# Optimization experiments

Measured on AMD Instinct MI355X. Metric: run time of the kernel, lower is better.

## Reference

```python
import jax, jax.numpy as jnp
import numpy as np

B, H, W, C = 8, 64, 64, 128
G = 8
K = 3
STRIDE, PAD, DIL = 1, 1, 1
OS = 1.0
HID = 2 * C
C_OUT = C
EPS = 1e-5


def setup_inputs():
    key = jax.random.key(0)
    ks = jax.random.split(key, 16)

    def n(k, shape, s=0.02):
        return jax.random.normal(k, shape, dtype=jnp.float32) * s

    inp = jax.random.normal(ks[0], (B, H, W, C), dtype=jnp.float32)
    return {
        "inp": inp,
        "w_proj": n(ks[1], (C, C), 0.05),
        "b_proj": jnp.zeros((C,), jnp.float32),
        "dw_w": n(ks[2], (C, 1, K, K), 0.1),
        "dw_b": jnp.zeros((C,), jnp.float32),
        "gamma": jnp.ones((C,), jnp.float32),
        "beta": jnp.zeros((C,), jnp.float32),
        "w_off": n(ks[3], (G * K * K * 2, C), 0.02),
        "b_off": n(ks[4], (G * K * K * 2,), 0.02),
        "w_mask": n(ks[5], (G * K * K, C), 0.02),
        "b_mask": n(ks[6], (G * K * K,), 0.02),
        "w_fc1": n(ks[7], (HID, C), 0.05),
        "b_fc1": jnp.zeros((HID,), jnp.float32),
        "w_fc2": n(ks[8], (C_OUT, HID), 0.05),
        "b_fc2": jnp.zeros((C_OUT,), jnp.float32),
    }


def _dcnv3_core(x, offset, mask):
    # x: (B,H,W,C); offset: (B,H,W,G*P*2); mask: (B,H,W,G*P), softmaxed over P
    b, h, w, c = x.shape
    cg = c // G
    p = K * K
    xpad = jnp.pad(x, ((0, 0), (PAD, PAD), (PAD, PAD), (0, 0)))
    hp, wp = h + 2 * PAD, w + 2 * PAD
    hout = (hp - (DIL * (K - 1) + 1)) // STRIDE + 1
    wout = (wp - (DIL * (K - 1) + 1)) // STRIDE + 1
    # reference points, normalized by padded spatial dims (DCNv3 convention)
    base = (DIL * (K - 1)) // 2 + 0.5
    ref_y = (base + jnp.arange(hout, dtype=x.dtype) * STRIDE) / hp
    ref_x = (base + jnp.arange(wout, dtype=x.dtype) * STRIDE) / wp
    # dilation kernel grid; flatten with p = i*K + j (row-major over kernel)
    k_lin = jnp.arange(K, dtype=x.dtype) * DIL - (DIL * (K - 1)) // 2
    grid_y = jnp.repeat(k_lin / hp, K)   # (P,)
    grid_x = jnp.tile(k_lin / wp, K)     # (P,)
    off = offset.reshape(b, hout, wout, G, p, 2)  # last dim = (dx, dy)
    loc_x = ref_x[None, None, :, None, None] + grid_x * OS + off[..., 0] * OS / wp
    loc_y = ref_y[None, :, None, None, None] + grid_y * OS + off[..., 1] * OS / hp
    # normalized [0,1] -> pixel coords (grid_sample align_corners=False)
    px = loc_x * wp - 0.5
    py = loc_y * hp - 0.5
    x0 = jnp.floor(px)
    y0 = jnp.floor(py)
    wx = px - x0
    wy = py - y0
    x0i = x0.astype(jnp.int32)
    y0i = y0.astype(jnp.int32)
    xg = xpad.reshape(b, hp * wp, G, cg).transpose(0, 2, 1, 3)  # (B,G,HpWp,Cg)
    m_tot = hout * wout * p

    def bgp(t):  # (B,Hout,Wout,G,P) -> (B,G,M,1)
        return t.transpose(0, 3, 1, 2, 4).reshape(b, G, m_tot)[..., None]

    def gather(iy, ix):
        valid = ((iy >= 0) & (iy < hp) & (ix >= 0) & (ix < wp)).astype(x.dtype)
        flat = jnp.clip(iy, 0, hp - 1) * wp + jnp.clip(ix, 0, wp - 1)
        v = jnp.take_along_axis(xg, bgp(flat), axis=2)  # (B,G,M,Cg)
        return v * bgp(valid)  # zero padding outside

    wxr, wyr = bgp(wx), bgp(wy)
    val = (gather(y0i, x0i) * (1 - wyr) * (1 - wxr)
           + gather(y0i, x0i + 1) * (1 - wyr) * wxr
           + gather(y0i + 1, x0i) * wyr * (1 - wxr)
           + gather(y0i + 1, x0i + 1) * wyr * wxr)
    m = bgp(mask.reshape(b, hout, wout, G, p))
    out = (val * m).reshape(b, G, hout * wout, p, cg).sum(3)  # (B,G,N,Cg)
    return out.transpose(0, 2, 1, 3).reshape(b, hout, wout, G * cg)


def reference(inp, w_proj, b_proj, dw_w, dw_b, gamma, beta, w_off, b_off,
              w_mask, b_mask, w_fc1, b_fc1, w_fc2, b_fc2):
    bsz = inp.shape[0]
    x = inp @ w_proj.T + b_proj  # input_proj
    # offset/mask branch: depthwise conv -> BN (batch stats) -> GELU
    xc = inp.transpose(0, 3, 1, 2)  # NCHW
    y = jax.lax.conv_general_dilated(
        xc, dw_w, (1, 1), [((K - 1) // 2, (K - 1) // 2)] * 2,
        feature_group_count=C, dimension_numbers=("NCHW", "OIHW", "NCHW"))
    y = y + dw_b[None, :, None, None]
    mean = y.mean(axis=(0, 2, 3), keepdims=True)
    var = ((y - mean) ** 2).mean(axis=(0, 2, 3), keepdims=True)
    y = (y - mean) * jax.lax.rsqrt(var + EPS)
    y = y * gamma[None, :, None, None] + beta[None, :, None, None]
    x1 = jax.nn.gelu(y, approximate=False).transpose(0, 2, 3, 1)  # (B,H,W,C)
    offset = x1 @ w_off.T + b_off
    mask = x1 @ w_mask.T + b_mask
    mask = jax.nn.softmax(mask.reshape(bsz, H, W, G, K * K), axis=-1).reshape(bsz, H, W, -1)
    x = _dcnv3_core(x, offset, mask)
    # out_proj MLP
    hdn = jax.nn.gelu(x @ w_fc1.T + b_fc1, approximate=False)
    out = hdn @ w_fc2.T + b_fc2
    return out.transpose(0, 3, 1, 2)  # (B,C_out,H,W)
```

## Files before the change

### kernel.cpp

```cpp
#include <hip/hip_runtime.h>
#include <math.h>

#define NPOS  32768
#define CDIM  128
#define HS    64
#define WSZ   64

typedef __bf16 bf8_t  __attribute__((ext_vector_type(8)));
typedef float  f32x4  __attribute__((ext_vector_type(4)));

__device__ __forceinline__ float gelu_exact(float x) {
    return 0.5f * x * (1.0f + erff(x * 0.70710678118654752f));
}

__device__ __forceinline__ unsigned short bf16c(float v) {
    return __builtin_bit_cast(unsigned short, (__bf16)v);
}

__device__ __forceinline__ uint4 pack8hi(const float* v) {
    unsigned hh[8];
    #pragma unroll
    for (int i = 0; i < 8; ++i) hh[i] = (unsigned)bf16c(v[i]);
    return make_uint4(hh[0] | (hh[1] << 16), hh[2] | (hh[3] << 16),
                      hh[4] | (hh[5] << 16), hh[6] | (hh[7] << 16));
}

__device__ __forceinline__ float bfd(unsigned u) {
    return __builtin_bit_cast(float, u << 16);
}

__device__ __forceinline__ void ufma(float* acc, uint4 c, float wgt) {
    const unsigned* cc = (const unsigned*)&c;
    #pragma unroll
    for (int j = 0; j < 4; ++j) {
        acc[2 * j]     += __builtin_bit_cast(float, cc[j] << 16) * wgt;
        acc[2 * j + 1] += __builtin_bit_cast(float, cc[j] & 0xFFFF0000u) * wgt;
    }
}


__device__ void prep_body(
    int bid, int tid,
    unsigned short* __restrict__ xpad,
    const float* __restrict__ w0, const float* __restrict__ w1,
    const float* __restrict__ w2, const float* __restrict__ w3,
    const float* __restrict__ w4, unsigned short* __restrict__ wb)
{
    if (bid < 130) {
        int idx = bid * 256 + tid;
        if (idx < 33280) {
            int c8 = (idx & 15) * 8;
            int cell = idx >> 4;
            int b = cell / 260, r = cell % 260;
            int h, w;
            if (r < 66)       { h = 0;  w = r; }
            else if (r < 132) { h = 65; w = r - 66; }
            else { int rr = r - 132; h = 1 + (rr >> 1); w = (rr & 1) * 65; }
            size_t o = (((size_t)b * 66 + h) * 66 + w) * 128 + c8;
            *(uint4*)(xpad + o) = make_uint4(0u, 0u, 0u, 0u);
        }
    } else {
        int sub = (bid - 130) * 4 + (tid >> 6);
        int lane = tid & 63;
        int NT, K, local; unsigned short* out; bool hl; bool comb = false;
        const float* W = nullptr; int N = 0;
        if (sub < 32)       { NT = 8;  K = 128; out = wb;          local = sub;       hl = false; W = w0; N = 128; }
        else if (sub < 88)  { NT = 14; K = 128; out = wb + 16384;  local = sub - 32;  hl = false; comb = true; }
        else if (sub < 152) { NT = 16; K = 128; out = wb + 45056;  local = sub - 88;  hl = true;  W = w3; N = 256; }
        else                { NT = 8;  K = 256; out = wb + 110592; local = sub - 152; hl = true;  W = w4; N = 128; }
        int KC = K / 32;
        int unit = KC * NT * 512;
        int kc = local / NT, t = local % NT;
        int nt = t * 16 + (lane & 15);
        const float* Wp = W; int n = nt, Nv = N;
        if (comb) {
            if (t < 9) { Wp = w1; n = nt;       Nv = 144; }
            else       { Wp = w2; n = nt - 144; Nv = 72;  }
        }
        int kb = kc * 32 + (lane >> 4) * 8;
        size_t base = ((size_t)local * 64 + lane) * 8;
        #pragma unroll
        for (int i = 0; i < 8; ++i) {
            float v = (n < Nv) ? Wp[(size_t)n * K + kb + i] : 0.f;
            __bf16 h = (__bf16)v;
            out[base + i] = __builtin_bit_cast(unsigned short, h);
            if (hl) {
                __bf16 l = (__bf16)(v - (float)h);
                out[unit + base + i] = __builtin_bit_cast(unsigned short, l);
            }
        }
    }
}

__device__ void dwconv_body(
    int blk, int tid,
    const float* __restrict__ inp, const float* __restrict__ dww,
    const float* __restrict__ dwb, unsigned short* __restrict__ ydwb,
    float* __restrict__ psum, float* __restrict__ psq,
    unsigned short* __restrict__ inpf)
{
    int b = blk >> 6, h = blk & 63;
    int c4 = (tid & 31) * 4;
    int wg = tid >> 5;

    float wreg[4][9];
    #pragma unroll
    for (int cc = 0; cc < 4; ++cc)
        #pragma unroll
        for (int p = 0; p < 9; ++p)
            wreg[cc][p] = dww[(c4 + cc) * 9 + p];
    float bia[4];
    #pragma unroll
    for (int cc = 0; cc < 4; ++cc) bia[cc] = dwb[c4 + cc];

    float s4[4] = {0,0,0,0}, q4[4] = {0,0,0,0};
    const float* ibase = inp + (size_t)(b << 12) * CDIM;

    for (int i = 0; i < 8; ++i) {
        int w = wg + i * 8;
        float acc[4] = {bia[0], bia[1], bia[2], bia[3]};
        float4 ctr;
        #pragma unroll
        for (int ky = 0; ky < 3; ++ky) {
            int yy = h + ky - 1;
            if (yy < 0 || yy >= HS) continue;
            #pragma unroll
            for (int kx = 0; kx < 3; ++kx) {
                int xx = w + kx - 1;
                if (xx < 0 || xx >= WSZ) continue;
                float4 v = *(const float4*)(ibase + (size_t)(yy * 64 + xx) * CDIM + c4);
                if (ky == 1 && kx == 1) ctr = v;
                int p = ky * 3 + kx;
                acc[0] += v.x * wreg[0][p];
                acc[1] += v.y * wreg[1][p];
                acc[2] += v.z * wreg[2][p];
                acc[3] += v.w * wreg[3][p];
            }
        }
        int r = (b << 12) + h * 64 + w;
        ushort4 o;
        o.x = bf16c(acc[0]); o.y = bf16c(acc[1]);
        o.z = bf16c(acc[2]); o.w = bf16c(acc[3]);
        *(ushort4*)(ydwb + (size_t)r * CDIM + c4) = o;
        {
            int rt = r >> 4, kc = c4 >> 5;
            int lp = (r & 15) + ((c4 & 31) >> 3) * 16;
            int i0 = c4 & 7;
            unsigned u0 = (unsigned)bf16c(ctr.x) | ((unsigned)bf16c(ctr.y) << 16);
            unsigned u1 = (unsigned)bf16c(ctr.z) | ((unsigned)bf16c(ctr.w) << 16);
            *(uint2*)(inpf + ((size_t)rt * 4 + kc) * 512 + lp * 8 + i0) = make_uint2(u0, u1);
        }
        #pragma unroll
        for (int cc = 0; cc < 4; ++cc) { s4[cc] += acc[cc]; q4[cc] += acc[cc] * acc[cc]; }
    }

    __shared__ float ls[8][128], lq[8][128];
    #pragma unroll
    for (int cc = 0; cc < 4; ++cc) { ls[wg][c4 + cc] = s4[cc]; lq[wg][c4 + cc] = q4[cc]; }
    __syncthreads();
    if (tid < 128) {
        float s = 0.f, q = 0.f;
        #pragma unroll
        for (int r = 0; r < 8; ++r) { s += ls[r][tid]; q += lq[r][tid]; }
        psum[blk * 128 + tid] = s;
        psq [blk * 128 + tid] = q;
    }
}

__global__ __launch_bounds__(256) void k_pd(
    const float* __restrict__ inp, unsigned short* __restrict__ inpf,
    unsigned short* __restrict__ xpad,
    const float* __restrict__ w0, const float* __restrict__ w1,
    const float* __restrict__ w2, const float* __restrict__ w3,
    const float* __restrict__ w4, unsigned short* __restrict__ wb,
    const float* __restrict__ dww, const float* __restrict__ dwb,
    unsigned short* __restrict__ ydwb, float* __restrict__ psum,
    float* __restrict__ psq)
{
    int bid = blockIdx.x;
    if (bid < 184) prep_body(bid, threadIdx.x, xpad, w0, w1, w2, w3, w4, wb);
    else           dwconv_body(bid - 184, threadIdx.x, inp, dww, dwb, ydwb, psum, psq, inpf);
}

__global__ __launch_bounds__(256) void k_bnstats(
    const float* __restrict__ psum, const float* __restrict__ psq,
    const float* __restrict__ gamma, const float* __restrict__ beta,
    float* __restrict__ sc, float* __restrict__ sh)
{
    int c = blockIdx.x;
    int t = threadIdx.x;
    float s = psum[t * 128 + c] + psum[(t + 256) * 128 + c];
    float q = psq [t * 128 + c] + psq [(t + 256) * 128 + c];
    __shared__ float rs[256], rq[256];
    rs[t] = s; rq[t] = q; __syncthreads();
    for (int off = 128; off > 0; off >>= 1) {
        if (t < off) { rs[t] += rs[t + off]; rq[t] += rq[t + off]; }
        __syncthreads();
    }
    if (t == 0) {
        float mean = rs[0] * (1.0f / 32768.0f);
        float var  = rq[0] * (1.0f / 32768.0f) - mean * mean;
        float scale = gamma[c] * rsqrtf(var + 1e-5f);
        sc[c] = scale;
        sh[c] = beta[c] - mean * scale;
    }
}

__device__ void bngelu_body(
    int bid, int tid,
    const unsigned short* __restrict__ ydwb, const float* __restrict__ sc,
    const float* __restrict__ sh, unsigned short* __restrict__ dst)
{
    int idx = bid * 256 + tid;
    int r = idx >> 4, k8 = (idx & 15) * 8;
    uint4 yv = *(const uint4*)(ydwb + (size_t)r * 128 + k8);
    const unsigned* cc = (const unsigned*)&yv;
    float t[8];
    #pragma unroll
    for (int j = 0; j < 4; ++j) {
        t[2 * j]     = bfd(cc[j]);
        t[2 * j + 1] = __builtin_bit_cast(float, cc[j] & 0xFFFF0000u);
    }
    float s[8], h[8];
    *(float4*)(s)     = *(const float4*)(sc + k8);
    *(float4*)(s + 4) = *(const float4*)(sc + k8 + 4);
    *(float4*)(h)     = *(const float4*)(sh + k8);
    *(float4*)(h + 4) = *(const float4*)(sh + k8 + 4);
    #pragma unroll
    for (int i = 0; i < 8; ++i) t[i] = gelu_exact(t[i] * s[i] + h[i]);
    uint4 hi = pack8hi(t);
    int rt = r >> 4, kc = k8 >> 5, lp = (r & 15) + ((k8 & 31) >> 3) * 16;
    size_t base = ((size_t)rt * 4 + kc) * 512 + lp * 8;
    *(uint4*)(dst + base) = hi;
}

template<int KDIM, int NT_TOT, int NT_W, int MODE, int NV>
__device__ void fgemm_body(
    int bx, int by, int tid,
    const unsigned short* __restrict__ AF, const unsigned short* __restrict__ WF,
    const float* __restrict__ bias, float* __restrict__ C,
    const float* __restrict__ bias2, float* __restrict__ C2)
{
    constexpr int KC = KDIM / 32;
    int lane = tid & 63, w = tid >> 6;
    int rt0 = bx * 8 + w * 2;
    int t0 = by * NT_W;

    f32x4 acc[2][NT_W];
    #pragma unroll
    for (int rt = 0; rt < 2; ++rt)
        #pragma unroll
        for (int t = 0; t < NT_W; ++t) acc[rt][t] = (f32x4){0.f, 0.f, 0.f, 0.f};

    const bf8_t* Ab0 = (const bf8_t*)AF + (size_t)rt0 * KC * 64 + lane;
    const bf8_t* Ab1 = Ab0 + KC * 64;
    const bf8_t* WHp = (const bf8_t*)WF + lane;

    #pragma unroll
    for (int kc = 0; kc < KC; ++kc) {
        bf8_t a0h = Ab0[kc * 64];
        bf8_t a1h = Ab1[kc * 64];
        #pragma unroll
        for (int t = 0; t < NT_W; ++t) {
            int tg = t0 + t;
            if (tg < NT_TOT) {
                bf8_t wh = WHp[(kc * NT_TOT + tg) * 64];
                acc[0][t] = __builtin_amdgcn_mfma_f32_16x16x32_bf16(wh, a0h, acc[0][t], 0, 0, 0);
                acc[1][t] = __builtin_amdgcn_mfma_f32_16x16x32_bf16(wh, a1h, acc[1][t], 0, 0, 0);
            }
        }
    }

    #pragma unroll
    for (int rt = 0; rt < 2; ++rt) {
        if (MODE == 3) {
            unsigned short* Cp = (unsigned short*)C;
            int m = (rt0 + rt) * 16 + (lane & 15);
            int bb_ = m >> 12, hwm = m & 4095;
            size_t rowb = (((size_t)bb_ * 66 + (hwm >> 6) + 1) * 66 + (hwm & 63) + 1) * 128;
            #pragma unroll
            for (int t = 0; t < NT_W; ++t) {
                int tg = t0 + t;
                int nb = tg * 16 + ((lane >> 4) << 2);
                if (tg < NT_TOT) {
                    float4 bb = *(const float4*)(bias + nb);
                    f32x4 a = acc[rt][t];
                    ushort4 v;
                    v.x = bf16c(a[0] + bb.x); v.y = bf16c(a[1] + bb.y);
                    v.z = bf16c(a[2] + bb.z); v.w = bf16c(a[3] + bb.w);
                    *(ushort4*)(Cp + rowb + nb) = v;
                }
            }
        } else if (MODE == 4) {
            unsigned short* Co = (unsigned short*)C;
            unsigned short* Cm = (unsigned short*)C2;
            int m = (rt0 + rt) * 16 + (lane & 15);
            #pragma unroll
            for (int t = 0; t < NT_W; ++t) {
                int tg = t0 + t;
                if (tg < NT_TOT) {
                    int nb = tg * 16 + ((lane >> 4) << 2);
                    f32x4 a = acc[rt][t];
                    if (nb < 144) {
                        float4 bb = *(const float4*)(bias + nb);
                        ushort4 v;
                        v.x = bf16c(a[0] + bb.x); v.y = bf16c(a[1] + bb.y);
                        v.z = bf16c(a[2] + bb.z); v.w = bf16c(a[3] + bb.w);
                        *(ushort4*)(Co + (size_t)m * 144 + nb) = v;
                    } else {
                        int col = nb - 144;
                        if (col + 4 <= 72) {
                            float4 bb = *(const float4*)(bias2 + col);
                            ushort4 v;
                            v.x = bf16c(a[0] + bb.x); v.y = bf16c(a[1] + bb.y);
                            v.z = bf16c(a[2] + bb.z); v.w = bf16c(a[3] + bb.w);
                            *(ushort4*)(Cm + (size_t)m * 72 + col) = v;
                        }
                    }
                }
            }
        }
    }
}

template<int KDIM, int NT_TOT, int NT_W, int MODE, int NV>
__global__ __launch_bounds__(256) void k_fgemm(
    const unsigned short* __restrict__ AF, const unsigned short* __restrict__ WF,
    const float* __restrict__ bias, float* __restrict__ C,
    const float* __restrict__ bias2, float* __restrict__ C2)
{
    fgemm_body<KDIM, NT_TOT, NT_W, MODE, NV>(
        blockIdx.x, blockIdx.y, threadIdx.x, AF, WF, bias, C, bias2, C2);
}

__global__ __launch_bounds__(256) void k_bp(
    const unsigned short* __restrict__ ydwb, const float* __restrict__ sc,
    const float* __restrict__ sh, unsigned short* __restrict__ x1f,
    const unsigned short* __restrict__ inpf, const unsigned short* __restrict__ wprojf,
    const float* __restrict__ bproj, unsigned short* __restrict__ xpad)
{
    int bid = blockIdx.x;
    if (bid < 2048) {
        bngelu_body(bid, threadIdx.x, ydwb, sc, sh, x1f);
    } else {
        int pbid = bid - 2048;
        fgemm_body<128, 8, 4, 3, 128>(pbid & 255, pbid >> 8, threadIdx.x,
            inpf, wprojf, bproj, (float*)xpad, nullptr, nullptr);
    }
}

__global__ __launch_bounds__(256) void k_dcn(
    const unsigned short* __restrict__ xpad, const unsigned short* __restrict__ offs,
    const unsigned short* __restrict__ msk, unsigned short* __restrict__ dcnf)
{
    int u = blockIdx.x * 256 + threadIdx.x;
    int g = u & 7;
    int pos = u >> 3;
    int b = pos >> 12, hw = pos & 4095, h = hw >> 6, w = hw & 63;

    const unsigned short* ml = msk + (size_t)pos * 72 + g * 9;
    float e[9];
    float mx = -1e30f;
    #pragma unroll
    for (int p = 0; p < 9; ++p) { e[p] = bfd((unsigned)ml[p]); mx = fmaxf(mx, e[p]); }
    float ssum = 0.f;
    #pragma unroll
    for (int p = 0; p < 9; ++p) { e[p] = __expf(e[p] - mx); ssum += e[p]; }
    float inv = 1.0f / ssum;

    const unsigned short* ob = offs + (size_t)pos * 144 + g * 18;
    const unsigned short* xb = xpad + (size_t)b * 557568 + g * 16;

    float acc[16];
    #pragma unroll
    for (int i = 0; i < 16; ++i) acc[i] = 0.f;

    #pragma unroll
    for (int p = 0; p < 9; ++p) {
        unsigned dpair = *(const unsigned*)(ob + p * 2);
        float dx = bfd(dpair);
        float dy = __builtin_bit_cast(float, dpair & 0xFFFF0000u);
        float px = (float)(w + (p % 3)) + dx;
        float py = (float)(h + (p / 3)) + dy;
        float x0f = floorf(px), y0f = floorf(py);
        float wx = px - x0f, wy = py - y0f;
        int ix = (int)x0f, iy = (int)y0f;
        int ix0 = max(min(ix, 65), 0),     ix1 = max(min(ix + 1, 65), 0);
        int iy0 = max(min(iy, 65), 0),     iy1 = max(min(iy + 1, 65), 0);
        int r0 = iy0 * 66, r1 = iy1 * 66;

        float mp  = e[p] * inv;
        float w11 = wy * wx * mp;
        float w10 = wy * mp - w11;
        float w01 = wx * mp - w11;
        float w00 = mp - w01 - w10 - w11;

        const unsigned short* c00 = xb + (size_t)(r0 + ix0) * 128;
        const unsigned short* c01 = xb + (size_t)(r0 + ix1) * 128;
        const unsigned short* c10 = xb + (size_t)(r1 + ix0) * 128;
        const unsigned short* c11 = xb + (size_t)(r1 + ix1) * 128;

        uint4 a00 = *(const uint4*)(c00), b00 = *(const uint4*)(c00 + 8);
        uint4 a01 = *(const uint4*)(c01), b01 = *(const uint4*)(c01 + 8);
        uint4 a10 = *(const uint4*)(c10), b10 = *(const uint4*)(c10 + 8);
        uint4 a11 = *(const uint4*)(c11), b11 = *(const uint4*)(c11 + 8);

        ufma(acc,     a00, w00); ufma(acc + 8, b00, w00);
        ufma(acc,     a01, w01); ufma(acc + 8, b01, w01);
        ufma(acc,     a10, w10); ufma(acc + 8, b10, w10);
        ufma(acc,     a11, w11); ufma(acc + 8, b11, w11);
    }

    int rt = pos >> 4, kc = g >> 1;
    int lp0 = (pos & 15) + (g & 1) * 32;
    size_t fb = ((size_t)rt * 4 + kc) * 512 + (size_t)lp0 * 8;
    uint4 hiA = pack8hi(acc);
    uint4 hiB = pack8hi(acc + 8);
    *(uint4*)(dcnf + fb)       = hiA;
    *(uint4*)(dcnf + fb + 128) = hiB;
}

__global__ __launch_bounds__(512) void k_mlp(
    const unsigned short* __restrict__ dcnf, const unsigned short* __restrict__ wf1,
    const float* __restrict__ bfc1, const unsigned short* __restrict__ wf2,
    const float* __restrict__ bfc2, float* __restrict__ out)
{
    __shared__ unsigned short hid[4][16][264];
    int tid = threadIdx.x;
    int lane = tid & 63, w = tid >> 6;
    int pr = w & 1, chunk = w >> 1;
    int bp = blockIdx.x * 2 + pr;
    int rt0 = bp * 2;
    int m = lane & 15, hi4 = (lane >> 4) << 2;

    f32x4 acc[2][4];
    #pragma unroll
    for (int r = 0; r < 2; ++r)
        #pragma unroll
        for (int t = 0; t < 4; ++t) acc[r][t] = (f32x4){0.f, 0.f, 0.f, 0.f};
    const bf8_t* Ab0 = (const bf8_t*)dcnf + (size_t)rt0 * 4 * 64 + lane;
    const bf8_t* Ab1 = Ab0 + 4 * 64;
    const bf8_t* WH1 = (const bf8_t*)wf1 + lane;
    #pragma unroll
    for (int kc = 0; kc < 4; ++kc) {
        bf8_t a0 = Ab0[kc * 64];
        bf8_t a1 = Ab1[kc * 64];
        #pragma unroll
        for (int t = 0; t < 4; ++t) {
            int tg = chunk * 4 + t;
            bf8_t wh = WH1[(kc * 16 + tg) * 64];
            acc[0][t] = __builtin_amdgcn_mfma_f32_16x16x32_bf16(wh, a0, acc[0][t], 0, 0, 0);
            acc[1][t] = __builtin_amdgcn_mfma_f32_16x16x32_bf16(wh, a1, acc[1][t], 0, 0, 0);
        }
    }
    #pragma unroll
    for (int r = 0; r < 2; ++r) {
        #pragma unroll
        for (int t = 0; t < 4; ++t) {
            int nb = (chunk * 4 + t) * 16 + hi4;
            float4 bb = *(const float4*)(bfc1 + nb);
            ushort4 v;
            v.x = bf16c(gelu_exact(acc[r][t][0] + bb.x));
            v.y = bf16c(gelu_exact(acc[r][t][1] + bb.y));
            v.z = bf16c(gelu_exact(acc[r][t][2] + bb.z));
            v.w = bf16c(gelu_exact(acc[r][t][3] + bb.w));
            *(ushort4*)(&hid[pr * 2 + r][m][nb]) = v;
        }
    }

    __syncthreads();

    f32x4 acc2[2][2];
    #pragma unroll
    for (int r = 0; r < 2; ++r)
        #pragma unroll
        for (int t = 0; t < 2; ++t) acc2[r][t] = (f32x4){0.f, 0.f, 0.f, 0.f};
    const bf8_t* WH2 = (const bf8_t*)wf2 + lane;
    #pragma unroll
    for (int kc = 0; kc < 8; ++kc) {
        bf8_t ah0 = *(const bf8_t*)(&hid[pr * 2 + 0][m][kc * 32 + (lane >> 4) * 8]);
        bf8_t ah1 = *(const bf8_t*)(&hid[pr * 2 + 1][m][kc * 32 + (lane >> 4) * 8]);
        #pragma unroll
        for (int t = 0; t < 2; ++t) {
            int tg = chunk * 2 + t;
            bf8_t wh = WH2[(kc * 8 + tg) * 64];
            acc2[0][t] = __builtin_amdgcn_mfma_f32_16x16x32_bf16(ah0, wh, acc2[0][t], 0, 0, 0);
            acc2[1][t] = __builtin_amdgcn_mfma_f32_16x16x32_bf16(ah1, wh, acc2[1][t], 0, 0, 0);
        }
    }
    #pragma unroll
    for (int r = 0; r < 2; ++r) {
        int m4 = (rt0 + r) * 16 + hi4;
        int b = m4 >> 12, hw = m4 & 4095;
        #pragma unroll
        for (int t = 0; t < 2; ++t) {
            int n = (chunk * 2 + t) * 16 + m;
            float bb = bfc2[n];
            f32x4 a = acc2[r][t];
            float4 v = {a[0] + bb, a[1] + bb, a[2] + bb, a[3] + bb};
            *(float4*)(out + (((size_t)(b * 128 + n)) << 12) + hw) = v;
        }
    }
}

extern "C" void kernel_launch(void* const* d_in, const int* in_sizes, int n_in,
                              void* d_out, int out_size, void* d_ws, size_t ws_size,
                              hipStream_t stream)
{
    const float* inp   = (const float*)d_in[0];
    const float* wproj = (const float*)d_in[1];
    const float* bproj = (const float*)d_in[2];
    const float* dww   = (const float*)d_in[3];
    const float* dwb   = (const float*)d_in[4];
    const float* gamma = (const float*)d_in[5];
    const float* beta  = (const float*)d_in[6];
    const float* woff  = (const float*)d_in[7];
    const float* boff  = (const float*)d_in[8];
    const float* wmask = (const float*)d_in[9];
    const float* bmask = (const float*)d_in[10];
    const float* wfc1  = (const float*)d_in[11];
    const float* bfc1  = (const float*)d_in[12];
    const float* wfc2  = (const float*)d_in[13];
    const float* bfc2  = (const float*)d_in[14];
    float* out = (float*)d_out;
    float* ws  = (float*)d_ws;

    unsigned short* xpad = (unsigned short*)ws;
    unsigned short* offs = (unsigned short*)(ws + 2230272);
    unsigned short* inpf  = (unsigned short*)(ws + 9179136);
    unsigned short* dcnf  = (unsigned short*)(ws + 9179136);
    unsigned short* x1f   = (unsigned short*)(ws + 13373440);
    unsigned short* ydwb  = (unsigned short*)(ws + 15470592);
    unsigned short* msk = (unsigned short*)(ws + 17567744);
    float* psum = ws + 19927040;
    float* psq  = ws + 19992576;
    float* scs  = ws + 20058112;
    float* shs  = ws + 20058240;
    unsigned short* wfr = (unsigned short*)(ws + 20058368);

    unsigned short* wproj_f = wfr;
    unsigned short* womb_f  = wfr + 16384;
    unsigned short* wfc1_f  = wfr + 45056;
    unsigned short* wfc2_f  = wfr + 110592;

    k_pd<<<696, 256, 0, stream>>>(inp, inpf, xpad, wproj, woff, wmask, wfc1, wfc2,
                                  wfr, dww, dwb, ydwb, psum, psq);
    k_bnstats<<<128, 256, 0, stream>>>(psum, psq, gamma, beta, scs, shs);
    k_bp<<<2560, 256, 0, stream>>>(ydwb, scs, shs, x1f, inpf, wproj_f, bproj, xpad);
    k_fgemm<128, 14, 4, 4, 224><<<dim3(256, 4), 256, 0, stream>>>(x1f, womb_f, boff, (float*)offs, bmask, (float*)msk);
    k_dcn<<<1024, 256, 0, stream>>>(xpad, offs, msk, dcnf);
    k_mlp<<<512, 512, 0, stream>>>(dcnf, wfc1_f, bfc1, wfc2_f, bfc2, out);
}
```

Before: 91.89 us.

## Fuse offset/mask projection GEMM into the DCN sampling kernel via shared memory

Removes the separate offset/mask GEMM launch and computes each block's 32 positions of offset and mask logits with MFMA inside k_dcn, staging them in LDS instead of writing to and rereading from global memory. This cuts one kernel launch and the global round-trip of the 216-wide bf16 offset/mask tensors. In exchange, each DCN block now does GEMM work before a __syncthreads, with 4 waves each computing 7 N-tiles, and uses extra LDS.

```diff
diff --git a/kernel.cpp b/kernel.cpp
--- a/kernel.cpp
+++ b/kernel.cpp
@@ -238,8 +238,7 @@
 __device__ void fgemm_body(
     int bx, int by, int tid,
     const unsigned short* __restrict__ AF, const unsigned short* __restrict__ WF,
-    const float* __restrict__ bias, float* __restrict__ C,
-    const float* __restrict__ bias2, float* __restrict__ C2)
+    const float* __restrict__ bias, float* __restrict__ C)
 {
     constexpr int KC = KDIM / 32;
     int lane = tid & 63, w = tid >> 6;
@@ -291,46 +290,8 @@
                     *(ushort4*)(Cp + rowb + nb) = v;
                 }
             }
-        } else if (MODE == 4) {
-            unsigned short* Co = (unsigned short*)C;
-            unsigned short* Cm = (unsigned short*)C2;
-            int m = (rt0 + rt) * 16 + (lane & 15);
-            #pragma unroll
-            for (int t = 0; t < NT_W; ++t) {
-                int tg = t0 + t;
-                if (tg < NT_TOT) {
-                    int nb = tg * 16 + ((lane >> 4) << 2);
-                    f32x4 a = acc[rt][t];
-                    if (nb < 144) {
-                        float4 bb = *(const float4*)(bias + nb);
-                        ushort4 v;
-                        v.x = bf16c(a[0] + bb.x); v.y = bf16c(a[1] + bb.y);
-                        v.z = bf16c(a[2] + bb.z); v.w = bf16c(a[3] + bb.w);
-                        *(ushort4*)(Co + (size_t)m * 144 + nb) = v;
-                    } else {
-                        int col = nb - 144;
-                        if (col + 4 <= 72) {
-                            float4 bb = *(const float4*)(bias2 + col);
-                            ushort4 v;
-                            v.x = bf16c(a[0] + bb.x); v.y = bf16c(a[1] + bb.y);
-                            v.z = bf16c(a[2] + bb.z); v.w = bf16c(a[3] + bb.w);
-                            *(ushort4*)(Cm + (size_t)m * 72 + col) = v;
-                        }
-                    }
-                }
-            }
-        }
-    }
-}
-
-template<int KDIM, int NT_TOT, int NT_W, int MODE, int NV>
-__global__ __launch_bounds__(256) void k_fgemm(
-    const unsigned short* __restrict__ AF, const unsigned short* __restrict__ WF,
-    const float* __restrict__ bias, float* __restrict__ C,
-    const float* __restrict__ bias2, float* __restrict__ C2)
-{
-    fgemm_body<KDIM, NT_TOT, NT_W, MODE, NV>(
-        blockIdx.x, blockIdx.y, threadIdx.x, AF, WF, bias, C, bias2, C2);
+        }
+    }
 }
 
 __global__ __launch_bounds__(256) void k_bp(
@@ -345,30 +306,78 @@
     } else {
         int pbid = bid - 2048;
         fgemm_body<128, 8, 4, 3, 128>(pbid & 255, pbid >> 8, threadIdx.x,
-            inpf, wprojf, bproj, (float*)xpad, nullptr, nullptr);
+            inpf, wprojf, bproj, (float*)xpad);
     }
 }
 
 __global__ __launch_bounds__(256) void k_dcn(
-    const unsigned short* __restrict__ xpad, const unsigned short* __restrict__ offs,
-    const unsigned short* __restrict__ msk, unsigned short* __restrict__ dcnf)
-{
-    int u = blockIdx.x * 256 + threadIdx.x;
-    int g = u & 7;
-    int pos = u >> 3;
+    const unsigned short* __restrict__ x1f, const unsigned short* __restrict__ womb,
+    const float* __restrict__ boff, const float* __restrict__ bmask,
+    const unsigned short* __restrict__ xpad, unsigned short* __restrict__ dcnf)
+{
+    __shared__ unsigned short offs_l[32][148];
+    __shared__ unsigned short msk_l[32][76];
+    int tid = threadIdx.x;
+    int lane = tid & 63, wv = tid >> 6;
+    int rtl = wv & 1, chunk = wv >> 1;
+    int rt = blockIdx.x * 2 + rtl;
+
+    {
+        f32x4 acc[7];
+        #pragma unroll
+        for (int t = 0; t < 7; ++t) acc[t] = (f32x4){0.f, 0.f, 0.f, 0.f};
+        const bf8_t* Ab = (const bf8_t*)x1f + (size_t)rt * 4 * 64 + lane;
+        const bf8_t* WH = (const bf8_t*)womb + lane;
+        #pragma unroll
+        for (int kc = 0; kc < 4; ++kc) {
+            bf8_t ah = Ab[kc * 64];
+            #pragma unroll
+            for (int t = 0; t < 7; ++t) {
+                int tg = chunk * 7 + t;
+                bf8_t wh = WH[(kc * 14 + tg) * 64];
+                acc[t] = __builtin_amdgcn_mfma_f32_16x16x32_bf16(wh, ah, acc[t], 0, 0, 0);
+            }
+        }
+        int m = rtl * 16 + (lane & 15);
+        #pragma unroll
+        for (int t = 0; t < 7; ++t) {
+            int tg = chunk * 7 + t;
+            int nb = tg * 16 + ((lane >> 4) << 2);
+            f32x4 a = acc[t];
+            if (nb < 144) {
+                float4 bb = *(const float4*)(boff + nb);
+                ushort4 v;
+                v.x = bf16c(a[0] + bb.x); v.y = bf16c(a[1] + bb.y);
+                v.z = bf16c(a[2] + bb.z); v.w = bf16c(a[3] + bb.w);
+                *(ushort4*)(&offs_l[m][nb]) = v;
+            } else {
+                int col = nb - 144;
+                if (col + 4 <= 72) {
+                    float4 bb = *(const float4*)(bmask + col);
+                    ushort4 v;
+                    v.x = bf16c(a[0] + bb.x); v.y = bf16c(a[1] + bb.y);
+                    v.z = bf16c(a[2] + bb.z); v.w = bf16c(a[3] + bb.w);
+                    *(ushort4*)(&msk_l[m][col]) = v;
+                }
+            }
+        }
+    }
+    __syncthreads();
+
+    int g = tid & 7;
+    int lpos = tid >> 3;
+    int pos = blockIdx.x * 32 + lpos;
     int b = pos >> 12, hw = pos & 4095, h = hw >> 6, w = hw & 63;
 
-    const unsigned short* ml = msk + (size_t)pos * 72 + g * 9;
     float e[9];
     float mx = -1e30f;
     #pragma unroll
-    for (int p = 0; p < 9; ++p) { e[p] = bfd((unsigned)ml[p]); mx = fmaxf(mx, e[p]); }
+    for (int p = 0; p < 9; ++p) { e[p] = bfd((unsigned)msk_l[lpos][g * 9 + p]); mx = fmaxf(mx, e[p]); }
     float ssum = 0.f;
     #pragma unroll
     for (int p = 0; p < 9; ++p) { e[p] = __expf(e[p] - mx); ssum += e[p]; }
     float inv = 1.0f / ssum;
 
-    const unsigned short* ob = offs + (size_t)pos * 144 + g * 18;
     const unsigned short* xb = xpad + (size_t)b * 557568 + g * 16;
 
     float acc[16];
@@ -377,7 +386,7 @@
 
     #pragma unroll
     for (int p = 0; p < 9; ++p) {
-        unsigned dpair = *(const unsigned*)(ob + p * 2);
+        unsigned dpair = *(const unsigned*)(&offs_l[lpos][g * 18 + p * 2]);
         float dx = bfd(dpair);
         float dy = __builtin_bit_cast(float, dpair & 0xFFFF0000u);
         float px = (float)(w + (p % 3)) + dx;
@@ -411,9 +420,9 @@
         ufma(acc,     a11, w11); ufma(acc + 8, b11, w11);
     }
 
-    int rt = pos >> 4, kc = g >> 1;
+    int rto = pos >> 4, kc = g >> 1;
     int lp0 = (pos & 15) + (g & 1) * 32;
-    size_t fb = ((size_t)rt * 4 + kc) * 512 + (size_t)lp0 * 8;
+    size_t fb = ((size_t)rto * 4 + kc) * 512 + (size_t)lp0 * 8;
     uint4 hiA = pack8hi(acc);
     uint4 hiB = pack8hi(acc + 8);
     *(uint4*)(dcnf + fb)       = hiA;
@@ -526,12 +535,10 @@
     float* ws  = (float*)d_ws;
 
     unsigned short* xpad = (unsigned short*)ws;
-    unsigned short* offs = (unsigned short*)(ws + 2230272);
     unsigned short* inpf  = (unsigned short*)(ws + 9179136);
     unsigned short* dcnf  = (unsigned short*)(ws + 9179136);
     unsigned short* x1f   = (unsigned short*)(ws + 13373440);
     unsigned short* ydwb  = (unsigned short*)(ws + 15470592);
-    unsigned short* msk = (unsigned short*)(ws + 17567744);
     float* psum = ws + 19927040;
     float* psq  = ws + 19992576;
     float* scs  = ws + 20058112;
@@ -547,7 +554,6 @@
                                   wfr, dww, dwb, ydwb, psum, psq);
     k_bnstats<<<128, 256, 0, stream>>>(psum, psq, gamma, beta, scs, shs);
     k_bp<<<2560, 256, 0, stream>>>(ydwb, scs, shs, x1f, inpf, wproj_f, bproj, xpad);
-    k_fgemm<128, 14, 4, 4, 224><<<dim3(256, 4), 256, 0, stream>>>(x1f, womb_f, boff, (float*)offs, bmask, (float*)msk);
-    k_dcn<<<1024, 256, 0, stream>>>(xpad, offs, msk, dcnf);
+    k_dcn<<<1024, 256, 0, stream>>>(x1f, womb_f, boff, bmask, xpad, dcnf);
     k_mlp<<<512, 512, 0, stream>>>(dcnf, wfc1_f, bfc1, wfc2_f, bfc2, out);
 }
```

New measurement: 85.95 us. 6.5% less time.
